# Optimization experiments

Measured on AMD Instinct MI355X. Metric: run time of the kernel, lower is better.

The kernel has to match this reference:

```python
import jax, jax.numpy as jnp
import numpy as np

N_HEAD = 16
WINDOW = 256
GLOBAL = 32


def _sparse_mask(T):
    # local window of +/- WINDOW//2 plus global rows/cols for first GLOBAL tokens
    i = jnp.arange(T)
    local = jnp.abs(i[:, None] - i[None, :]) <= (WINDOW // 2)
    glob = (i[:, None] < GLOBAL) | (i[None, :] < GLOBAL)
    return local | glob  # [T, T] bool


def setup_inputs() -> dict:
    key = jax.random.key(0)
    k1, k2, k3 = jax.random.split(key, 3)
    B, T, C = 1, 4096, 1024
    scale = 0.02
    return {
        "x": jax.random.normal(k1, (B, T, C), dtype=jnp.float32),
        "W_attn": jax.random.normal(k2, (C, 3 * C), dtype=jnp.float32) * scale,
        "b_attn": jnp.zeros((3 * C,), dtype=jnp.float32),
        "W_proj": jax.random.normal(k3, (C, C), dtype=jnp.float32) * scale,
        "b_proj": jnp.zeros((C,), dtype=jnp.float32),
    }


def reference(x, W_attn, b_attn, W_proj, b_proj):
    B, T, C = x.shape
    H = N_HEAD
    D = C // H

    qkv = x @ W_attn + b_attn  # [B, T, 3C]
    q, k, v = jnp.split(qkv, 3, axis=-1)
    # [B, H, T, D]
    q = q.reshape(B, T, H, D).transpose(0, 2, 1, 3)
    k = k.reshape(B, T, H, D).transpose(0, 2, 1, 3)
    v = v.reshape(B, T, H, D).transpose(0, 2, 1, 3)

    mask = _sparse_mask(T)  # [T, T]
    att = jnp.einsum("bhqd,bhkd->bhqk", q, k) * (1.0 / np.sqrt(D))
    neg = jnp.finfo(att.dtype).min
    att = jnp.where(mask, att, neg)
    att = jax.nn.softmax(att, axis=-1)
    y = jnp.einsum("bhqk,bhkd->bhqd", att, v)  # [B, H, T, D]
    y = y.transpose(0, 2, 1, 3).reshape(B, T, C)
    return y @ W_proj + b_proj
```

## Files before the change

### kernel.cpp

```cpp
#include <hip/hip_runtime.h>
#include <hip/hip_bf16.h>
#include <math.h>

#define T_SEQ 4096
#define C_DIM 1024
#define H_HEADS 16
#define D_HEAD 64
#define QKVW 3072
#define WIN_HALF 128
#define GLOBAL_TOK 32

typedef __attribute__((ext_vector_type(8))) short bf16x8;
typedef __attribute__((ext_vector_type(4))) float f32x4;

__device__ __forceinline__ float bf2f(unsigned short u) {
    union { unsigned int i; float f; } c; c.i = ((unsigned int)u) << 16; return c.f;
}
__device__ __forceinline__ unsigned short f2bf(float f) {
    union { float f; unsigned int i; } c; c.f = f;
    return (unsigned short)((c.i + 0x7fffu + ((c.i >> 16) & 1u)) >> 16);
}

__device__ __forceinline__ void gll16(const unsigned short* g, unsigned short* l) {
    __builtin_amdgcn_global_load_lds(
        (const __attribute__((address_space(1))) void*)g,
        (__attribute__((address_space(3))) void*)l, 16, 0, 0);
}

__device__ __forceinline__ int swz(int row, int chunk) {
    return row * 64 + ((chunk ^ (row & 7)) * 8);
}

__global__ __launch_bounds__(256) void prep_kernel(
    const float* __restrict__ x, const float* __restrict__ Wa,
    const float* __restrict__ Wp,
    unsigned short* __restrict__ xb, unsigned short* __restrict__ Wabt,
    unsigned short* __restrict__ Wpbt)
{
    __shared__ unsigned short tile[32][36];
    const int bid = blockIdx.x;
    const int t = threadIdx.x;
    if (bid < 4096) {
        const int idx = bid * 256 + t;
        float4 v = ((const float4*)x)[idx];
        ushort4 o;
        o.x = f2bf(v.x); o.y = f2bf(v.y); o.z = f2bf(v.z); o.w = f2bf(v.w);
        ((ushort4*)xb)[idx] = o;
        return;
    }
    const float* src; unsigned short* dst; int R, Ncols, bx, by;
    if (bid < 4096 + 3072) {
        const int b = bid - 4096;
        src = Wa; dst = Wabt; R = C_DIM; Ncols = QKVW;
        bx = b % (QKVW / 32); by = b / (QKVW / 32);
    } else {
        const int b = bid - 7168;
        src = Wp; dst = Wpbt; R = C_DIM; Ncols = C_DIM;
        bx = b % (C_DIM / 32); by = b / (C_DIM / 32);
    }
    const int r0 = by * 32, c0 = bx * 32;
    const int rr = t >> 3, cq = (t & 7) * 4;
    float4 v = *(const float4*)(src + (size_t)(r0 + rr) * Ncols + c0 + cq);
    tile[rr][cq + 0] = f2bf(v.x); tile[rr][cq + 1] = f2bf(v.y);
    tile[rr][cq + 2] = f2bf(v.z); tile[rr][cq + 3] = f2bf(v.w);
    __syncthreads();
    const int cc = t >> 3, rq = (t & 7) * 4;
    ushort4 o;
    o.x = tile[rq + 0][cc]; o.y = tile[rq + 1][cc];
    o.z = tile[rq + 2][cc]; o.w = tile[rq + 3][cc];
    *(ushort4*)(dst + (size_t)(c0 + cc) * R + r0 + rq) = o;
}

#define GBK 64
template<int OUT_BF16, int WRITE_VT>
__device__ __forceinline__ void gemm_body(
    const unsigned short* __restrict__ A,
    const unsigned short* __restrict__ Bt,
    const float* __restrict__ bias,
    void* __restrict__ Cv, unsigned short* __restrict__ vTp,
    int M, int N, int K)
{
    __shared__ unsigned short As[128 * GBK];
    __shared__ unsigned short Bs[128 * GBK];
    const int tid = threadIdx.x;
    const int w = tid >> 6, lane = tid & 63;
    const int quad = lane >> 4, r16 = lane & 15;
    const int m0 = blockIdx.y * 128, n0 = blockIdx.x * 128;
    const int wm = (w & 1) * 64, wn = (w >> 1) * 64;
    const int sr = lane >> 3;
    const int sc8 = ((lane & 7) ^ sr) * 8;

    f32x4 acc[4][4];
    #pragma unroll
    for (int i = 0; i < 4; ++i)
        #pragma unroll
        for (int j = 0; j < 4; ++j) acc[i][j] = (f32x4){0.f, 0.f, 0.f, 0.f};

    const unsigned short* Ab = A + (size_t)m0 * K;
    const unsigned short* Bb = Bt + (size_t)n0 * K;

    for (int k0 = 0; k0 < K; k0 += GBK) {
        __syncthreads();
        #pragma unroll
        for (int i = 0; i < 4; ++i) {
            const int r = w * 32 + i * 8 + sr;
            gll16(Ab + (size_t)r * K + k0 + sc8, &As[(w * 32 + i * 8) * GBK]);
            gll16(Bb + (size_t)r * K + k0 + sc8, &Bs[(w * 32 + i * 8) * GBK]);
        }
        asm volatile("s_waitcnt vmcnt(0)" ::: "memory");
        __builtin_amdgcn_sched_barrier(0);
        __syncthreads();

        #pragma unroll
        for (int kk = 0; kk < 2; ++kk) {
            bf16x8 af[4], bf_[4];
            #pragma unroll
            for (int t = 0; t < 4; ++t) {
                const int ra = wm + t * 16 + r16;
                af[t]  = *(const bf16x8*)&As[ra * GBK + (((kk * 4 + quad) ^ (ra & 7)) * 8)];
                const int rb = wn + t * 16 + r16;
                bf_[t] = *(const bf16x8*)&Bs[rb * GBK + (((kk * 4 + quad) ^ (rb & 7)) * 8)];
            }
            #pragma unroll
            for (int mt = 0; mt < 4; ++mt)
                #pragma unroll
                for (int nt = 0; nt < 4; ++nt)
                    acc[mt][nt] = __builtin_amdgcn_mfma_f32_16x16x32_bf16(
                        af[mt], bf_[nt], acc[mt][nt], 0, 0, 0);
        }
    }

    if (WRITE_VT && n0 >= 2 * C_DIM) {
        #pragma unroll
        for (int nt = 0; nt < 4; ++nt) {
            const int col = n0 + wn + nt * 16 + r16;
            const float bv = bias[col];
            const int vcol = col - 2 * C_DIM;
            #pragma unroll
            for (int mt = 0; mt < 4; ++mt) {
                ushort4 o;
                o.x = f2bf(acc[mt][nt][0] + bv);
                o.y = f2bf(acc[mt][nt][1] + bv);
                o.z = f2bf(acc[mt][nt][2] + bv);
                o.w = f2bf(acc[mt][nt][3] + bv);
                *(ushort4*)&vTp[(size_t)vcol * T_SEQ + m0 + wm + mt * 16 + quad * 4] = o;
            }
        }
    } else {
        #pragma unroll
        for (int nt = 0; nt < 4; ++nt) {
            const int col = n0 + wn + nt * 16 + r16;
            const float bv = bias[col];
            #pragma unroll
            for (int mt = 0; mt < 4; ++mt)
                #pragma unroll
                for (int reg = 0; reg < 4; ++reg) {
                    const int row = m0 + wm + mt * 16 + quad * 4 + reg;
                    if (OUT_BF16)
                        ((unsigned short*)Cv)[(size_t)row * N + col] = f2bf(acc[mt][nt][reg] + bv);
                    else
                        ((float*)Cv)[(size_t)row * N + col] = acc[mt][nt][reg] + bv;
                }
        }
    }
}

__global__ __launch_bounds__(256) void gemm_qkv_kernel(
    const unsigned short* __restrict__ A, const unsigned short* __restrict__ Bt,
    const float* __restrict__ bias, void* __restrict__ Cv,
    unsigned short* __restrict__ vTp, int M, int N, int K)
{
    gemm_body<1, 1>(A, Bt, bias, Cv, vTp, M, N, K);
}
__global__ __launch_bounds__(256) void gemm_proj_kernel(
    const unsigned short* __restrict__ A, const unsigned short* __restrict__ Bt,
    const float* __restrict__ bias, void* __restrict__ Cv,
    unsigned short* __restrict__ vTp, int M, int N, int K)
{
    gemm_body<0, 0>(A, Bt, bias, Cv, vTp, M, N, K);
}

#define PT_STRIDE 72
#define NSLOT 8
#define PROW 72

struct KVbuf { bf16x8 kl[4], kh[4], vl[4], vh[4]; };
struct StReg { bf16x8 a, b, c, d; };

#define LOAD_KV(C0, B)                                                         \
  {                                                                            \
    const unsigned short* kr_ = kb + (size_t)((C0) + n) * QKVW + quad * 8;     \
    _Pragma("unroll")                                                          \
    for (int g = 0; g < 4; ++g) {                                              \
      B.kl[g] = *(const bf16x8*)(kr_ + (size_t)(g * 16) * QKVW);               \
      B.kh[g] = *(const bf16x8*)(kr_ + (size_t)(g * 16) * QKVW + 32);          \
    }                                                                          \
    const unsigned short* vr_ = vb + (size_t)n * T_SEQ + (C0) + quad * 8;      \
    _Pragma("unroll")                                                          \
    for (int d = 0; d < 4; ++d) {                                              \
      B.vl[d] = *(const bf16x8*)(vr_ + (size_t)(d * 16) * T_SEQ);              \
      B.vh[d] = *(const bf16x8*)(vr_ + (size_t)(d * 16) * T_SEQ + 32);         \
    }                                                                          \
  }

#define SOFTMAX_P_UPDATE(StV)                                                  \
    mm = fmaxf(mm, __shfl_xor(mm, 16));                                        \
    mm = fmaxf(mm, __shfl_xor(mm, 32));                                        \
    const float mn = fmaxf(m_run, mm);                                         \
    const float mnf = (mn == -INFINITY) ? 0.f : mn;                            \
    const float al = __expf(m_run - mnf);                                      \
    float rs = 0.f;                                                            \
    _Pragma("unroll")                                                          \
    for (int g = 0; g < 4; ++g) {                                              \
      const float e0 = __expf(StV[g][0] - mnf);                                \
      const float e1 = __expf(StV[g][1] - mnf);                                \
      const float e2 = __expf(StV[g][2] - mnf);                                \
      const float e3 = __expf(StV[g][3] - mnf);                                \
      rs += (e0 + e1) + (e2 + e3);                                             \
      const unsigned int p01 = f2bf(e0) | ((unsigned int)f2bf(e1) << 16);      \
      const unsigned int p23 = f2bf(e2) | ((unsigned int)f2bf(e3) << 16);      \
      *(unsigned int*)&myPt[n * PT_STRIDE + g * 16 + quad * 4] = p01;          \
      *(unsigned int*)&myPt[n * PT_STRIDE + g * 16 + quad * 4 + 2] = p23;      \
    }                                                                          \
    rs += __shfl_xor(rs, 16);                                                  \
    rs += __shfl_xor(rs, 32);                                                  \
    l_run = l_run * al + rs;                                                   \
    m_run = mn;                                                                \
    _Pragma("unroll")                                                          \
    for (int d = 0; d < 4; ++d)                                                \
      _Pragma("unroll")                                                        \
      for (int r = 0; r < 4; ++r) O[d][r] *= al;

#define PROC_TILE(ITV, CUR, NXT)                                               \
  {                                                                            \
    const int it_ = (ITV);                                                     \
    const int c0 = split * 512 + it_ * 64;                                     \
    f32x4 St[4];                                                               \
    __builtin_amdgcn_s_setprio(1);                                             \
    _Pragma("unroll")                                                          \
    for (int g = 0; g < 4; ++g) {                                              \
      St[g] = __builtin_amdgcn_mfma_f32_16x16x32_bf16(CUR.kl[g], q0, Zf, 0, 0, 0); \
      St[g] = __builtin_amdgcn_mfma_f32_16x16x32_bf16(CUR.kh[g], q1, St[g], 0, 0, 0); \
    }                                                                          \
    __builtin_amdgcn_s_setprio(0);                                             \
    if (it_ + 1 < n_tiles) {                                                   \
      LOAD_KV(c0 + 64, NXT);                                                   \
    }                                                                          \
    float mm = -INFINITY;                                                      \
    _Pragma("unroll")                                                          \
    for (int g = 0; g < 4; ++g)                                                \
      _Pragma("unroll")                                                        \
      for (int r = 0; r < 4; ++r) {                                            \
        const float v = St[g][r] * 0.125f;                                     \
        St[g][r] = v; mm = fmaxf(mm, v);                                       \
      }                                                                        \
    SOFTMAX_P_UPDATE(St)                                                       \
    asm volatile("s_waitcnt lgkmcnt(0)" ::: "memory");                         \
    __builtin_amdgcn_sched_barrier(0);                                         \
    __builtin_amdgcn_s_setprio(1);                                             \
    _Pragma("unroll")                                                          \
    for (int kg = 0; kg < 2; ++kg) {                                           \
      bf16x8 pf_ = *(const bf16x8*)&myPt[n * PT_STRIDE + kg * 32 + quad * 8];  \
      _Pragma("unroll")                                                        \
      for (int d = 0; d < 4; ++d)                                              \
        O[d] = __builtin_amdgcn_mfma_f32_16x16x32_bf16(                        \
            kg ? CUR.vh[d] : CUR.vl[d], pf_, O[d], 0, 0, 0);                   \
    }                                                                          \
    __builtin_amdgcn_s_setprio(0);                                             \
  }

#define STAGE_LOAD(C0, R)                                                      \
  { const int c0s_ = (C0);                                                     \
    R.a = *(const bf16x8*)(kb + (size_t)(c0s_ + srow) * QKVW + scol * 8);      \
    R.b = *(const bf16x8*)(kb + (size_t)(c0s_ + srow + 32) * QKVW + scol * 8); \
    R.c = *(const bf16x8*)(vb + (size_t)srow * T_SEQ + c0s_ + scol * 8);       \
    R.d = *(const bf16x8*)(vb + (size_t)(srow + 32) * T_SEQ + c0s_ + scol * 8); }

#define STAGE_WRITE(BUF, R)                                                    \
  { *(bf16x8*)&Ks[BUF][kdst0] = R.a;                                           \
    *(bf16x8*)&Ks[BUF][kdst1] = R.b;                                           \
    *(bf16x8*)&Vs[BUF][kdst0] = R.c;                                           \
    *(bf16x8*)&Vs[BUF][kdst1] = R.d; }

#define WTILE(ITV, BUF, RW, RL)                                                \
  {                                                                            \
    const int it_ = (ITV);                                                     \
    const int c0 = (it_ == 0) ? 0 : (blo + (it_ - 1) * 64);                    \
    if (activeW) {                                                             \
      bf16x8 kl[4], kh[4];                                                     \
      _Pragma("unroll")                                                        \
      for (int g = 0; g < 4; ++g) {                                            \
        kl[g] = *(const bf16x8*)&Ks[BUF][swz(n + g * 16, quad)];               \
        kh[g] = *(const bf16x8*)&Ks[BUF][swz(n + g * 16, quad + 4)];           \
      }                                                                        \
      f32x4 St[4];                                                             \
      __builtin_amdgcn_s_setprio(1);                                           \
      _Pragma("unroll")                                                        \
      for (int g = 0; g < 4; ++g) {                                            \
        St[g] = __builtin_amdgcn_mfma_f32_16x16x32_bf16(kl[g], q0, Zf, 0, 0, 0); \
        St[g] = __builtin_amdgcn_mfma_f32_16x16x32_bf16(kh[g], q1, St[g], 0, 0, 0); \
      }                                                                        \
      __builtin_amdgcn_s_setprio(0);                                           \
      float mm = -INFINITY;                                                    \
      if (it_ != 0 && c0 >= rowbase - 113 && c0 <= rowbase + 65) {             \
        _Pragma("unroll")                                                      \
        for (int g = 0; g < 4; ++g)                                            \
          _Pragma("unroll")                                                    \
          for (int r = 0; r < 4; ++r) {                                        \
            const float v = St[g][r] * 0.125f;                                 \
            St[g][r] = v; mm = fmaxf(mm, v);                                   \
          }                                                                    \
      } else if (it_ == 0 && rowbase >= 192) {                                 \
        _Pragma("unroll")                                                      \
        for (int g = 0; g < 2; ++g)                                            \
          _Pragma("unroll")                                                    \
          for (int r = 0; r < 4; ++r) {                                        \
            const float v = St[g][r] * 0.125f;                                 \
            St[g][r] = v; mm = fmaxf(mm, v);                                   \
          }                                                                    \
        _Pragma("unroll")                                                      \
        for (int g = 2; g < 4; ++g)                                            \
          _Pragma("unroll")                                                    \
          for (int r = 0; r < 4; ++r) St[g][r] = -INFINITY;                    \
      } else {                                                                 \
        _Pragma("unroll")                                                      \
        for (int g = 0; g < 4; ++g)                                            \
          _Pragma("unroll")                                                    \
          for (int r = 0; r < 4; ++r) {                                        \
            float v = St[g][r] * 0.125f;                                       \
            const int col = c0 + g * 16 + quad * 4 + r;                        \
            int dd = row - col; dd = dd < 0 ? -dd : dd;                        \
            if (!(col < GLOBAL_TOK || dd <= WIN_HALF)) v = -INFINITY;          \
            St[g][r] = v; mm = fmaxf(mm, v);                                   \
          }                                                                    \
      }                                                                        \
      SOFTMAX_P_UPDATE(St)                                                     \
      bf16x8 vl[4], vh[4];                                                     \
      _Pragma("unroll")                                                        \
      for (int d = 0; d < 4; ++d) {                                            \
        vl[d] = *(const bf16x8*)&Vs[BUF][swz(n + d * 16, quad)];               \
        vh[d] = *(const bf16x8*)&Vs[BUF][swz(n + d * 16, quad + 4)];           \
      }                                                                        \
      asm volatile("s_waitcnt lgkmcnt(0)" ::: "memory");                       \
      __builtin_amdgcn_sched_barrier(0);                                       \
      __builtin_amdgcn_s_setprio(1);                                           \
      _Pragma("unroll")                                                        \
      for (int kg = 0; kg < 2; ++kg) {                                         \
        bf16x8 pf_ = *(const bf16x8*)&myPt[n * PT_STRIDE + kg * 32 + quad * 8];\
        _Pragma("unroll")                                                      \
        for (int d = 0; d < 4; ++d)                                            \
          O[d] = __builtin_amdgcn_mfma_f32_16x16x32_bf16(                      \
              kg ? vh[d] : vl[d], pf_, O[d], 0, 0, 0);                         \
      }                                                                        \
      __builtin_amdgcn_s_setprio(0);                                           \
    }                                                                          \
    if (it_ + 1 < NT) {                                                        \
      asm volatile("s_waitcnt vmcnt(0)" ::: "memory");                         \
      __builtin_amdgcn_sched_barrier(0);                                       \
      STAGE_WRITE((BUF) ^ 1, RW);                                              \
      if (it_ + 2 < NT) { STAGE_LOAD(blo + (it_ + 1) * 64, RL); }              \
      __syncthreads();                                                         \
    }                                                                          \
  }

__global__ __launch_bounds__(256, 3) void sparse_attn_mfma(
    const unsigned short* __restrict__ qkv,
    const unsigned short* __restrict__ vT,
    unsigned short* __restrict__ y,
    float* __restrict__ part)
{
    __shared__ unsigned short Ks[2][64 * 64];
    __shared__ unsigned short Vs[2][64 * 64];
    __shared__ unsigned short Pt[4][16 * PT_STRIDE];
    const int tid = threadIdx.x;
    const int w = tid >> 6, lane = tid & 63;
    const int quad = lane >> 4, n = lane & 15;
    const int bid = blockIdx.x;
    const f32x4 Zf = (f32x4){0.f, 0.f, 0.f, 0.f};

    if (bid < 1024) {
        const int h = bid & 15;
        const int B = bid >> 4;
        const int base = B * 64;
        const int rowbase = base + w * 16;
        const bool activeW = !(B == 0 && w < 2);
        int blo = base - 128; if (blo < 64) blo = 64;
        int bhi = base + 192; if (bhi > T_SEQ) bhi = T_SEQ;
        const int NT = 1 + (bhi - blo) / 64;

        const unsigned short* kb = qkv + C_DIM + h * 64;
        const unsigned short* vb = vT + (size_t)h * 64 * T_SEQ;
        unsigned short* myPt = Pt[w];

        const int srow = tid >> 3, scol = tid & 7;
        const int kdst0 = swz(srow, scol);
        const int kdst1 = kdst0 + 32 * 64;

        const unsigned short* qp = qkv + (size_t)(rowbase + n) * QKVW + h * 64 + quad * 8;
        bf16x8 q0 = *(const bf16x8*)qp;
        bf16x8 q1 = *(const bf16x8*)(qp + 32);

        f32x4 O[4];
        #pragma unroll
        for (int i = 0; i < 4; ++i) O[i] = (f32x4){0.f, 0.f, 0.f, 0.f};
        float m_run = -INFINITY, l_run = 0.f;
        const int row = rowbase + n;

        StReg r0, r1;
        STAGE_LOAD(0, r0);
        asm volatile("s_waitcnt vmcnt(0)" ::: "memory");
        __builtin_amdgcn_sched_barrier(0);
        STAGE_WRITE(0, r0);
        STAGE_LOAD(blo, r1);
        __syncthreads();

        int it = 0;
        for (;;) {
            WTILE(it, 0, r1, r0);
            if (++it >= NT) break;
            WTILE(it, 1, r0, r1);
            if (++it >= NT) break;
        }

        if (activeW) {
            const float invL = 1.f / l_run;
            #pragma unroll
            for (int dblk = 0; dblk < 4; ++dblk)
                #pragma unroll
                for (int r = 0; r < 4; ++r)
                    y[(size_t)row * C_DIM + h * 64 + dblk * 16 + quad * 4 + r] =
                        f2bf(O[dblk][r] * invL);
        }
    } else {
        const int idx = bid - 1024;
        const int h = idx & 15;
        const int u = (idx >> 4) * 4 + w;
        const int rt = u >> 3, split = u & 7;
        const int rowbase = rt * 16;
        const int n_tiles = 8;

        const unsigned short* qp = qkv + (size_t)(rowbase + n) * QKVW + h * 64 + quad * 8;
        bf16x8 q0 = *(const bf16x8*)qp;
        bf16x8 q1 = *(const bf16x8*)(qp + 32);

        const unsigned short* kb = qkv + C_DIM + h * 64;
        const unsigned short* vb = vT + (size_t)h * 64 * T_SEQ;
        unsigned short* myPt = Pt[w];

        f32x4 O[4];
        #pragma unroll
        for (int i = 0; i < 4; ++i) O[i] = (f32x4){0.f, 0.f, 0.f, 0.f};
        float m_run = -INFINITY, l_run = 0.f;

        KVbuf b0, b1;
        LOAD_KV(split * 512, b0);
        int it = 0;
        for (;;) {
            PROC_TILE(it, b0, b1);
            if (++it >= n_tiles) break;
            PROC_TILE(it, b1, b0);
            if (++it >= n_tiles) break;
        }

        float* pb = part + ((size_t)(h * 2 + rt) * NSLOT + split) * 16 * PROW;
        #pragma unroll
        for (int dblk = 0; dblk < 4; ++dblk)
            #pragma unroll
            for (int r = 0; r < 4; ++r)
                pb[n * PROW + dblk * 16 + quad * 4 + r] = O[dblk][r];
        if (quad == 0) {
            pb[n * PROW + 64] = m_run;
            pb[n * PROW + 65] = l_run;
        }
    }
}

__global__ __launch_bounds__(64) void attn_combine(
    const float* __restrict__ part, unsigned short* __restrict__ y)
{
    const int d = threadIdx.x;
    const int h = blockIdx.x >> 1, rt = blockIdx.x & 1;
    const float* base = part + (size_t)(h * 2 + rt) * NSLOT * 16 * PROW;
    for (int row = 0; row < 16; ++row) {
        float M = -INFINITY;
        for (int sl = 0; sl < NSLOT; ++sl)
            M = fmaxf(M, base[(size_t)sl * 16 * PROW + row * PROW + 64]);
        float L = 0.f, Od = 0.f;
        for (int sl = 0; sl < NSLOT; ++sl) {
            const float* p = base + (size_t)sl * 16 * PROW + row * PROW;
            const float s = __expf(p[64] - M);
            L += p[65] * s;
            Od += p[d] * s;
        }
        y[(size_t)(rt * 16 + row) * C_DIM + h * 64 + d] = f2bf(Od / L);
    }
}

extern "C" void kernel_launch(void* const* d_in, const int* in_sizes, int n_in,
                              void* d_out, int out_size, void* d_ws, size_t ws_size,
                              hipStream_t stream) {
    const float* x  = (const float*)d_in[0];
    const float* Wa = (const float*)d_in[1];
    const float* ba = (const float*)d_in[2];
    const float* Wp = (const float*)d_in[3];
    const float* bp = (const float*)d_in[4];
    float* out = (float*)d_out;

    unsigned short* xb   = (unsigned short*)d_ws;
    unsigned short* Wabt = xb   + (size_t)T_SEQ * C_DIM;
    unsigned short* Wpbt = Wabt + (size_t)C_DIM * QKVW;
    unsigned short* qkv  = Wpbt + (size_t)C_DIM * C_DIM;
    unsigned short* yat  = qkv  + (size_t)T_SEQ * QKVW;
    unsigned short* vT   = yat  + (size_t)T_SEQ * C_DIM;
    float* part = (float*)(vT + (size_t)C_DIM * T_SEQ);

    prep_kernel<<<4096 + 3072 + 1024, 256, 0, stream>>>(
        x, Wa, Wp, xb, Wabt, Wpbt);

    gemm_qkv_kernel<<<dim3(QKVW / 128, T_SEQ / 128), 256, 0, stream>>>(
        xb, Wabt, ba, qkv, vT, T_SEQ, QKVW, C_DIM);

    const int nBlocks = 1024 + 64;
    sparse_attn_mfma<<<nBlocks, 256, 0, stream>>>(qkv, vT, yat, part);
    attn_combine<<<H_HEADS * 2, 64, 0, stream>>>(part, yat);

    gemm_proj_kernel<<<dim3(C_DIM / 128, T_SEQ / 128), 256, 0, stream>>>(
        yat, Wpbt, bp, out, nullptr, T_SEQ, C_DIM, C_DIM);
}
```

Before: 194.4 us.

## Double-buffer GEMM LDS tiles to overlap global loads with MFMA compute

The bf16 GEMM now keeps two LDS buffers for A and B and prefetches the tile two steps ahead using global_load_lds. It waits with vmcnt(8) so only the current stage has to land. The intent is to hide global memory latency behind the MFMA work instead of draining every load before each k-step. It doubles LDS use to 64KB per block, which may lower occupancy, and adds an extra barrier per iteration.

```diff
diff --git a/kernel.cpp b/kernel.cpp
--- a/kernel.cpp
+++ b/kernel.cpp
@@ -72,6 +72,14 @@
 }
 
 #define GBK 64
+#define GSTAGE(BUF, KO)                                                        \
+  _Pragma("unroll")                                                            \
+  for (int i = 0; i < 4; ++i) {                                                \
+    const int r = w * 32 + i * 8 + sr;                                         \
+    gll16(Ab + (size_t)r * K + (KO) + sc8, &As[BUF][(w * 32 + i * 8) * GBK]);  \
+    gll16(Bb + (size_t)r * K + (KO) + sc8, &Bs[BUF][(w * 32 + i * 8) * GBK]);  \
+  }
+
 template<int OUT_BF16, int WRITE_VT>
 __device__ __forceinline__ void gemm_body(
     const unsigned short* __restrict__ A,
@@ -80,8 +88,8 @@
     void* __restrict__ Cv, unsigned short* __restrict__ vTp,
     int M, int N, int K)
 {
-    __shared__ unsigned short As[128 * GBK];
-    __shared__ unsigned short Bs[128 * GBK];
+    __shared__ unsigned short As[2][128 * GBK];
+    __shared__ unsigned short Bs[2][128 * GBK];
     const int tid = threadIdx.x;
     const int w = tid >> 6, lane = tid & 63;
     const int quad = lane >> 4, r16 = lane & 15;
@@ -99,27 +107,25 @@
     const unsigned short* Ab = A + (size_t)m0 * K;
     const unsigned short* Bb = Bt + (size_t)n0 * K;
 
-    for (int k0 = 0; k0 < K; k0 += GBK) {
-        __syncthreads();
-        #pragma unroll
-        for (int i = 0; i < 4; ++i) {
-            const int r = w * 32 + i * 8 + sr;
-            gll16(Ab + (size_t)r * K + k0 + sc8, &As[(w * 32 + i * 8) * GBK]);
-            gll16(Bb + (size_t)r * K + k0 + sc8, &Bs[(w * 32 + i * 8) * GBK]);
-        }
-        asm volatile("s_waitcnt vmcnt(0)" ::: "memory");
+    const int NS = K / GBK;
+    GSTAGE(0, 0);
+    GSTAGE(1, GBK);
+
+    for (int t = 0; t < NS; ++t) {
+        if (t == NS - 1) { asm volatile("s_waitcnt vmcnt(0)" ::: "memory"); }
+        else             { asm volatile("s_waitcnt vmcnt(8)" ::: "memory"); }
         __builtin_amdgcn_sched_barrier(0);
         __syncthreads();
-
+        const int cb = t & 1;
         #pragma unroll
         for (int kk = 0; kk < 2; ++kk) {
             bf16x8 af[4], bf_[4];
             #pragma unroll
-            for (int t = 0; t < 4; ++t) {
-                const int ra = wm + t * 16 + r16;
-                af[t]  = *(const bf16x8*)&As[ra * GBK + (((kk * 4 + quad) ^ (ra & 7)) * 8)];
-                const int rb = wn + t * 16 + r16;
-                bf_[t] = *(const bf16x8*)&Bs[rb * GBK + (((kk * 4 + quad) ^ (rb & 7)) * 8)];
+            for (int tt = 0; tt < 4; ++tt) {
+                const int ra = wm + tt * 16 + r16;
+                af[tt]  = *(const bf16x8*)&As[cb][ra * GBK + (((kk * 4 + quad) ^ (ra & 7)) * 8)];
+                const int rb = wn + tt * 16 + r16;
+                bf_[tt] = *(const bf16x8*)&Bs[cb][rb * GBK + (((kk * 4 + quad) ^ (rb & 7)) * 8)];
             }
             #pragma unroll
             for (int mt = 0; mt < 4; ++mt)
@@ -127,6 +133,10 @@
                 for (int nt = 0; nt < 4; ++nt)
                     acc[mt][nt] = __builtin_amdgcn_mfma_f32_16x16x32_bf16(
                         af[mt], bf_[nt], acc[mt][nt], 0, 0, 0);
+        }
+        if (t + 2 < NS) {
+            __syncthreads();
+            GSTAGE(cb, (t + 2) * GBK);
         }
     }
 
```

Result: no change. 192.1 us (-1.2%).
